# Kernel tuning notes

Hardware: AMD Instinct MI355X
Metric: run time of the kernel (lower is better)

Reference implementation:

```python
import jax, jax.numpy as jnp
import numpy as np

# FineMatching constants (from init_kwargs)
GRID_NUM = 8
VOXEL = 0.04
NDIM = 3
MAX_NEIGHBORS = 128
OFFSET = GRID_NUM * VOXEL / 2.0           # 0.16
RADIUS = (GRID_NUM + 1) * VOXEL / 2.0      # 0.18
G1 = GRID_NUM + 1                          # grid nodes per dim
G = G1 ** NDIM                             # 729 flattened voxel bins
NEG_BIG = -1e30


def setup_inputs() -> dict:
    key = jax.random.key(0)
    k1, k2, k3, k4, k5 = jax.random.split(key, 5)
    B, L0, L1, C = 4, 2048, 2048, 64
    x0 = jax.random.normal(k1, (B, L0, C), dtype=jnp.float32)
    x1 = jax.random.normal(k2, (B, L1, C), dtype=jnp.float32)
    pos0 = jax.random.uniform(k3, (B, L0, 3), dtype=jnp.float32)
    pos1 = jax.random.uniform(k4, (B, L1, 3), dtype=jnp.float32)
    pad_mask = jax.random.uniform(k5, (B, L1)) < 0.1  # True = padded / masked out
    return {"x0": x0, "x1": x1, "pos0": pos0, "pos1": pos1, "pad_mask": pad_mask}


def reference(x0, x1, pos0, pos1, pad_mask):
    B, L0, C = x0.shape
    K = MAX_NEIGHBORS
    # --- radius neighbor search (per batch, dense distances, K nearest) ---
    d2 = jnp.sum((pos0[:, :, None, :] - pos1[:, None, :, :]) ** 2, axis=-1)  # (B,L0,L1)
    neg_d2, idx = jax.lax.top_k(-d2, K)                                       # (B,L0,K)
    valid = (-neg_d2) < RADIUS ** 2                                           # within radius
    pad_g = jnp.take_along_axis(pad_mask[:, None, :], idx, axis=2)           # (B,L0,K)
    valid = valid & (~pad_g)
    # --- edge-wise gather + correlation ---
    x1g = jnp.take_along_axis(x1[:, None, :, :], idx[..., None], axis=2)     # (B,L0,K,C)
    corr = jnp.einsum('blc,blkc->blk', x0, x1g) / jnp.sqrt(jnp.float32(C))
    # --- masked segment softmax over neighbors (nan -> 0 when no valid edge) ---
    logits = jnp.where(valid, corr, NEG_BIG)
    prob = jax.nn.softmax(logits, axis=-1) * valid                            # (B,L0,K)
    # --- flow aggregation ---
    pos1g = jnp.take_along_axis(pos1[:, None, :, :], idx[..., None], axis=2) # (B,L0,K,3)
    dpos = pos1g - pos0[:, :, None, :]
    flow = jnp.einsum('blk,blkd->bld', prob, dpos)                            # (B,L0,3)
    # --- P2G voxel scatter: bin prob mass into (grid_num+1)^3 voxel grid ---
    coords = (dpos + OFFSET) / VOXEL
    vox = jnp.clip(jnp.round(coords), 0, GRID_NUM).astype(jnp.int32)          # (B,L0,K,3)
    flat = (vox[..., 0] * G1 + vox[..., 1]) * G1 + vox[..., 2]                # (B,L0,K)
    b_ix = jnp.arange(B)[:, None, None]
    l_ix = jnp.arange(L0)[None, :, None]
    flow_dist = jnp.zeros((B, L0, G), dtype=x0.dtype).at[b_ix, l_ix, flat].add(prob)
    return flow, flow_dist
```

## Files before the change

### kernel.cpp

```cpp
#include <hip/hip_runtime.h>
#include <stdint.h>

#define NB    4
#define NL0   2048
#define NL1   2048
#define NC    64
#define KMAX  128
#define CAP   256
#define NG1   9
#define NBINS 729
#define FLOWN (NB*NL0*3)
#define QPB   8
#define TPB   512

__global__ __launch_bounds__(TPB, 8) void fine_match_kernel(
    const float* __restrict__ x0, const float* __restrict__ x1,
    const float* __restrict__ pos0, const float* __restrict__ pos1,
    const void* __restrict__ padraw, float* __restrict__ out)
{
  __shared__ float          s_x0[QPB*NC];
  __shared__ float          s_p0[QPB][3];
  __shared__ unsigned short s_jj[QPB][CAP];
  __shared__ float          s_corr[QPB][CAP];

  const int t = threadIdx.x;
  const int bid = blockIdx.x;
  const int b = bid >> 8;
  const int l0base = (bid & 255) * QPB;

  int wide;
  {
    const uint32_t* pi = (const uint32_t*)padraw;
    int ok4 = 1;
    for (int i = t; i < (NB*NL1)/4; i += TPB) {
      const uint32_t v = pi[i];
      ok4 &= (int)((v <= 1u) | (v == 0x3F800000u));
    }
    wide = __syncthreads_and(ok4);
  }

  s_x0[t] = x0[(size_t)(b*NL0 + l0base)*NC + t];
  if (t < QPB*3) {
    const int q = t/3, c = t - q*3;
    s_p0[q][c] = pos0[(b*NL0 + l0base + q)*3 + c];
  }
  {
    float4 z4; z4.x = z4.y = z4.z = z4.w = 0.0f;
    float4* bz = (float4*)(out + FLOWN + (size_t)(b*NL0 + l0base)*NBINS);
    for (int i = t; i < QPB*NBINS/4; i += TPB) bz[i] = z4;
  }
  __syncthreads();

  const int wv = t >> 6, lane = t & 63;
  const int l0 = l0base + wv;
  const float p0x = s_p0[wv][0], p0y = s_p0[wv][1], p0z = s_p0[wv][2];
  const float* pb = pos1 + (size_t)b*NL1*3;

  int cnt = 0;
  for (int base = 0; base < NL1; base += 64) {
    const int j = base + lane;
    const float dx = __fsub_rn(pb[j*3+0], p0x);
    const float dy = __fsub_rn(pb[j*3+1], p0y);
    const float dz = __fsub_rn(pb[j*3+2], p0z);
    const float d2 = __fadd_rn(__fadd_rn(__fmul_rn(dx,dx), __fmul_rn(dy,dy)), __fmul_rn(dz,dz));
    const bool ok = d2 < 0.0324f;
    const uint64_t m = __ballot(ok);
    if (ok) {
      const int pos = cnt + (int)__popcll(m & ((1ull << lane) - 1ull));
      if (pos < CAP) s_jj[wv][pos] = (unsigned short)j;
    }
    cnt += (int)__popcll(m);
  }
  if (cnt > CAP) cnt = CAP;
  __syncthreads();

  const bool over = (cnt > KMAX);
  for (int s = 0; s < 4; ++s) {
    if (64*s >= cnt) break;
    const int i = lane + 64*s;
    if (i < cnt) {
      float c = -1e30f;
      const int j = (int)s_jj[wv][i];
      bool k;
      if (wide) k = (((const uint32_t*)padraw)[b*NL1 + j] == 0u);
      else      k = (((const uint8_t*)padraw)[b*NL1 + j] == 0);
      if (over && k) {
        const float dx = __fsub_rn(pb[j*3+0], p0x);
        const float dy = __fsub_rn(pb[j*3+1], p0y);
        const float dz = __fsub_rn(pb[j*3+2], p0z);
        const float di = __fadd_rn(__fadd_rn(__fmul_rn(dx,dx), __fmul_rn(dy,dy)), __fmul_rn(dz,dz));
        int rank = 0;
        for (int m2 = 0; m2 < cnt; ++m2) {
          const int jm = (int)s_jj[wv][m2];
          const float ex = __fsub_rn(pb[jm*3+0], p0x);
          const float ey = __fsub_rn(pb[jm*3+1], p0y);
          const float ez = __fsub_rn(pb[jm*3+2], p0z);
          const float dm = __fadd_rn(__fadd_rn(__fmul_rn(ex,ex), __fmul_rn(ey,ey)), __fmul_rn(ez,ez));
          rank += (dm < di || (dm == di && m2 < i)) ? 1 : 0;
        }
        if (rank >= KMAX) k = false;
      }
      if (k) {
        const float* xr = x1 + ((size_t)b*NL1 + j)*NC;
        float acc = 0.0f;
        #pragma unroll
        for (int cc = 0; cc < NC; cc += 4) {
          const float4 v = *(const float4*)(xr + cc);
          const float4 q = *(const float4*)(&s_x0[wv*NC + cc]);
          acc += q.x*v.x + q.y*v.y + q.z*v.z + q.w*v.w;
        }
        c = acc * 0.125f;
      }
      s_corr[wv][i] = c;
    }
  }

  float mx = -1e30f;
  for (int s = 0; s < 4; ++s) {
    if (64*s >= cnt) break;
    const int i = lane + 64*s;
    if (i < cnt) { const float c = s_corr[wv][i]; if (c > mx) mx = c; }
  }
  for (int off = 32; off; off >>= 1) { const float o = __shfl_xor(mx, off); if (o > mx) mx = o; }
  float sum = 0.0f;
  for (int s = 0; s < 4; ++s) {
    if (64*s >= cnt) break;
    const int i = lane + 64*s;
    if (i < cnt) { const float c = s_corr[wv][i]; if (c > -1e30f) sum += expf(c - mx); }
  }
  for (int off = 32; off; off >>= 1) sum += __shfl_xor(sum, off);
  const float inv = (sum > 0.0f) ? (1.0f / sum) : 0.0f;

  float* bins = out + FLOWN + (size_t)((size_t)b*NL0 + l0)*NBINS;
  float fx = 0.0f, fy = 0.0f, fz = 0.0f;
  for (int s = 0; s < 4; ++s) {
    if (64*s >= cnt) break;
    const int i = lane + 64*s;
    if (i < cnt) {
      const float c = s_corr[wv][i];
      if (c > -1e30f) {
        const float pv = expf(c - mx) * inv;
        const int j = (int)s_jj[wv][i];
        const float dx = __fsub_rn(pb[j*3+0], p0x);
        const float dy = __fsub_rn(pb[j*3+1], p0y);
        const float dz = __fsub_rn(pb[j*3+2], p0z);
        fx += pv*dx; fy += pv*dy; fz += pv*dz;
        const float cx = __fdiv_rn(__fadd_rn(dx, 0.16f), 0.04f);
        const float cy = __fdiv_rn(__fadd_rn(dy, 0.16f), 0.04f);
        const float cz = __fdiv_rn(__fadd_rn(dz, 0.16f), 0.04f);
        int vx = (int)rintf(cx); vx = vx < 0 ? 0 : (vx > 8 ? 8 : vx);
        int vy = (int)rintf(cy); vy = vy < 0 ? 0 : (vy > 8 ? 8 : vy);
        int vz = (int)rintf(cz); vz = vz < 0 ? 0 : (vz > 8 ? 8 : vz);
        __hip_atomic_fetch_add(&bins[(vx*NG1 + vy)*NG1 + vz], pv,
                               __ATOMIC_RELAXED, __HIP_MEMORY_SCOPE_WORKGROUP);
      }
    }
  }
  for (int off = 32; off; off >>= 1) {
    fx += __shfl_xor(fx, off); fy += __shfl_xor(fy, off); fz += __shfl_xor(fz, off);
  }
  if (lane == 0) {
    float* f = out + (size_t)((size_t)b*NL0 + l0)*3;
    f[0] = fx; f[1] = fy; f[2] = fz;
  }
}

extern "C" void kernel_launch(void* const* d_in, const int* in_sizes, int n_in,
                              void* d_out, int out_size, void* d_ws, size_t ws_size,
                              hipStream_t stream) {
  const float* x0   = (const float*)d_in[0];
  const float* x1   = (const float*)d_in[1];
  const float* pos0 = (const float*)d_in[2];
  const float* pos1 = (const float*)d_in[3];
  const void*  pad  = d_in[4];
  float* out = (float*)d_out;
  (void)in_sizes; (void)n_in; (void)out_size; (void)d_ws; (void)ws_size;
  hipLaunchKernelGGL(fine_match_kernel, dim3(NB*NL0/QPB), dim3(TPB), 0, stream,
                     x0, x1, pos0, pos1, pad, out);
}
```

Measured before the change: 34.30 us.

## Accumulate voxel bins in LDS per wave and drop block-wide syncs

Each wave now builds its own query's 729-bin histogram in shared memory with LDS atomics, then writes it to global once with coalesced stores. This replaces the upfront zero-fill of the global output and the global atomics on it. Per-wave loading of x0 and pos0 removes two __syncthreads, so waves run independently after the pad-format check. The candidate cap drops from 256 to 192 to make room for the extra LDS, which could truncate neighbours if more than 192 fall inside the radius and may reduce occupancy.

```diff
diff --git a/kernel.cpp b/kernel.cpp
--- a/kernel.cpp
+++ b/kernel.cpp
@@ -6,9 +6,11 @@
 #define NL1   2048
 #define NC    64
 #define KMAX  128
-#define CAP   256
+#define CAP   192
+#define NSLOT 3
 #define NG1   9
 #define NBINS 729
+#define BINP  732
 #define FLOWN (NB*NL0*3)
 #define QPB   8
 #define TPB   512
@@ -19,9 +21,9 @@
     const void* __restrict__ padraw, float* __restrict__ out)
 {
   __shared__ float          s_x0[QPB*NC];
-  __shared__ float          s_p0[QPB][3];
   __shared__ unsigned short s_jj[QPB][CAP];
   __shared__ float          s_corr[QPB][CAP];
+  __shared__ float          s_bins[QPB][BINP];
 
   const int t = threadIdx.x;
   const int bid = blockIdx.x;
@@ -39,21 +41,14 @@
     wide = __syncthreads_and(ok4);
   }
 
-  s_x0[t] = x0[(size_t)(b*NL0 + l0base)*NC + t];
-  if (t < QPB*3) {
-    const int q = t/3, c = t - q*3;
-    s_p0[q][c] = pos0[(b*NL0 + l0base + q)*3 + c];
-  }
-  {
-    float4 z4; z4.x = z4.y = z4.z = z4.w = 0.0f;
-    float4* bz = (float4*)(out + FLOWN + (size_t)(b*NL0 + l0base)*NBINS);
-    for (int i = t; i < QPB*NBINS/4; i += TPB) bz[i] = z4;
-  }
-  __syncthreads();
-
   const int wv = t >> 6, lane = t & 63;
   const int l0 = l0base + wv;
-  const float p0x = s_p0[wv][0], p0y = s_p0[wv][1], p0z = s_p0[wv][2];
+
+  for (int i = lane; i < BINP; i += 64) s_bins[wv][i] = 0.0f;
+  s_x0[wv*NC + lane] = x0[(size_t)(b*NL0 + l0)*NC + lane];
+
+  const float* pq = pos0 + (size_t)(b*NL0 + l0)*3;
+  const float p0x = pq[0], p0y = pq[1], p0z = pq[2];
   const float* pb = pos1 + (size_t)b*NL1*3;
 
   int cnt = 0;
@@ -72,10 +67,9 @@
     cnt += (int)__popcll(m);
   }
   if (cnt > CAP) cnt = CAP;
-  __syncthreads();
 
   const bool over = (cnt > KMAX);
-  for (int s = 0; s < 4; ++s) {
+  for (int s = 0; s < NSLOT; ++s) {
     if (64*s >= cnt) break;
     const int i = lane + 64*s;
     if (i < cnt) {
@@ -116,14 +110,14 @@
   }
 
   float mx = -1e30f;
-  for (int s = 0; s < 4; ++s) {
+  for (int s = 0; s < NSLOT; ++s) {
     if (64*s >= cnt) break;
     const int i = lane + 64*s;
     if (i < cnt) { const float c = s_corr[wv][i]; if (c > mx) mx = c; }
   }
   for (int off = 32; off; off >>= 1) { const float o = __shfl_xor(mx, off); if (o > mx) mx = o; }
   float sum = 0.0f;
-  for (int s = 0; s < 4; ++s) {
+  for (int s = 0; s < NSLOT; ++s) {
     if (64*s >= cnt) break;
     const int i = lane + 64*s;
     if (i < cnt) { const float c = s_corr[wv][i]; if (c > -1e30f) sum += expf(c - mx); }
@@ -131,9 +125,8 @@
   for (int off = 32; off; off >>= 1) sum += __shfl_xor(sum, off);
   const float inv = (sum > 0.0f) ? (1.0f / sum) : 0.0f;
 
-  float* bins = out + FLOWN + (size_t)((size_t)b*NL0 + l0)*NBINS;
   float fx = 0.0f, fy = 0.0f, fz = 0.0f;
-  for (int s = 0; s < 4; ++s) {
+  for (int s = 0; s < NSLOT; ++s) {
     if (64*s >= cnt) break;
     const int i = lane + 64*s;
     if (i < cnt) {
@@ -151,8 +144,7 @@
         int vx = (int)rintf(cx); vx = vx < 0 ? 0 : (vx > 8 ? 8 : vx);
         int vy = (int)rintf(cy); vy = vy < 0 ? 0 : (vy > 8 ? 8 : vy);
         int vz = (int)rintf(cz); vz = vz < 0 ? 0 : (vz > 8 ? 8 : vz);
-        __hip_atomic_fetch_add(&bins[(vx*NG1 + vy)*NG1 + vz], pv,
-                               __ATOMIC_RELAXED, __HIP_MEMORY_SCOPE_WORKGROUP);
+        atomicAdd(&s_bins[wv][(vx*NG1 + vy)*NG1 + vz], pv);
       }
     }
   }
@@ -163,6 +155,9 @@
     float* f = out + (size_t)((size_t)b*NL0 + l0)*3;
     f[0] = fx; f[1] = fy; f[2] = fz;
   }
+
+  float* fd = out + FLOWN + (size_t)((size_t)b*NL0 + l0)*NBINS;
+  for (int i = lane; i < NBINS; i += 64) fd[i] = s_bins[wv][i];
 }
 
 extern "C" void kernel_launch(void* const* d_in, const int* in_sizes, int n_in,
```

Measured after the change: 32.57 us. -5.1%, faster.
